# Kernel optimization log

Hardware: AMD Instinct MI355X
Metric: run time of the kernel (lower is better)

Reference implementation:

```python
import jax, jax.numpy as jnp
from jax import lax
import numpy as np

B, T, D, H, C = 256, 2048, 40, 128, 35
LN_EPS = 1e-5


def _uniform(key, shape, scale):
    return jax.random.uniform(key, shape, jnp.float32, -scale, scale)


def setup_inputs() -> dict:
    key = jax.random.key(0)
    ks = jax.random.split(key, 16)
    s = 1.0 / np.sqrt(H)  # PyTorch LSTM init scale
    inp = {
        "x": jax.random.normal(ks[0], (B, T, D), jnp.float32),
        "length": jax.random.randint(ks[1], (B,), 1, T + 1, jnp.int32),
        # layer 0 (input_size=D)
        "W_ih0": _uniform(ks[2], (4 * H, D), s),
        "W_hh0": _uniform(ks[3], (4 * H, H), s),
        "b_ih0": _uniform(ks[4], (4 * H,), s),
        "b_hh0": _uniform(ks[5], (4 * H,), s),
        # layer 1 (input_size=H)
        "W_ih1": _uniform(ks[6], (4 * H, H), s),
        "W_hh1": _uniform(ks[7], (4 * H, H), s),
        "b_ih1": _uniform(ks[8], (4 * H,), s),
        "b_hh1": _uniform(ks[9], (4 * H,), s),
        # LayerNorm + Linear head
        "ln_gamma": jnp.ones((H,), jnp.float32),
        "ln_beta": jnp.zeros((H,), jnp.float32),
        "fc_w": _uniform(ks[10], (C, H), 1.0 / np.sqrt(H)),
        "fc_b": _uniform(ks[11], (C,), 1.0 / np.sqrt(H)),
    }
    return inp


def _lstm_layer(xs, length, W_ih, W_hh, b_ih, b_hh):
    # xs: [T, B, D_in]; masked recurrence emulates pack_padded_sequence:
    # state is frozen for t >= length, so the final h equals the state at
    # each sequence's last valid step.
    Tn, Bn = xs.shape[0], xs.shape[1]
    Hn = W_hh.shape[1]
    h0 = jnp.zeros((Bn, Hn), xs.dtype)
    c0 = jnp.zeros((Bn, Hn), xs.dtype)

    def step(carry, inp):
        h, c = carry
        x_t, t = inp
        gates = x_t @ W_ih.T + b_ih + h @ W_hh.T + b_hh  # [B, 4H]
        i, f, g, o = jnp.split(gates, 4, axis=-1)  # PyTorch gate order i,f,g,o
        i = jax.nn.sigmoid(i)
        f = jax.nn.sigmoid(f)
        g = jnp.tanh(g)
        o = jax.nn.sigmoid(o)
        c_new = f * c + i * g
        h_new = o * jnp.tanh(c_new)
        m = (t < length)[:, None]
        h = jnp.where(m, h_new, h)
        c = jnp.where(m, c_new, c)
        return (h, c), h

    (h_fin, c_fin), hs = lax.scan(step, (h0, c0), (xs, jnp.arange(Tn)))
    return hs, h_fin


def reference(x, length, W_ih0, W_hh0, b_ih0, b_hh0, W_ih1, W_hh1, b_ih1, b_hh1,
              ln_gamma, ln_beta, fc_w, fc_b):
    xs = jnp.transpose(x, (1, 0, 2))  # [T, B, D]
    hs1, _ = _lstm_layer(xs, length, W_ih0, W_hh0, b_ih0, b_hh0)
    _, h_last = _lstm_layer(hs1, length, W_ih1, W_hh1, b_ih1, b_hh1)  # h[-1]: [B, H]
    # LayerNorm over feature dim
    mu = jnp.mean(h_last, axis=-1, keepdims=True)
    var = jnp.mean(jnp.square(h_last - mu), axis=-1, keepdims=True)
    hn = (h_last - mu) * lax.rsqrt(var + LN_EPS) * ln_gamma + ln_beta
    return hn @ fc_w.T + fc_b  # [B, C]
```

## Files before the change

kernel.cpp:

```cpp
#include <hip/hip_runtime.h>

#define Bn 256
#define Tn 2048
#define Dn 40
#define Hn 128
#define Cn 35

typedef _Float16 h2 __attribute__((ext_vector_type(2)));

__device__ __forceinline__ int sdot4(int a, int b, int c) {
#if __has_builtin(__builtin_amdgcn_sdot4)
  return __builtin_amdgcn_sdot4(a, b, c, false);
#else
  int r = c;
#pragma unroll
  for (int i = 0; i < 4; ++i)
    r += ((int)(a << (24 - 8 * i)) >> 24) * ((int)(b << (24 - 8 * i)) >> 24);
  return r;
#endif
}

__device__ __forceinline__ float fdot2f(h2 a, h2 b, float c) {
#if __has_builtin(__builtin_amdgcn_fdot2)
  return __builtin_amdgcn_fdot2(a, b, c, false);
#else
  return c + (float)(a[0]) * (float)(b[0]) + (float)(a[1]) * (float)(b[1]);
#endif
}

__device__ __forceinline__ h2 bch(int u) { return __builtin_bit_cast(h2, u); }

__device__ __forceinline__ int pk2i(float a, float b) {
  h2 r; r[0] = (_Float16)a; r[1] = (_Float16)b;
  return __builtin_bit_cast(int, r);
}

__device__ __forceinline__ float rcpf_(float x) {
#if __has_builtin(__builtin_amdgcn_rcpf)
  return __builtin_amdgcn_rcpf(x);
#else
  return 1.f / x;
#endif
}

__device__ __forceinline__ float sigm(float v) {
  v = fmaxf(fminf(v, 60.f), -60.f);
  return rcpf_(1.f + __expf(-v));
}

__device__ __forceinline__ float tanha(float v) {
  v = fmaxf(fminf(v, 15.f), -15.f);
  const float e = __expf(2.f * v);
  return (e - 1.f) * rcpf_(e + 1.f);
}

__device__ __forceinline__ int q8c(float v) {
  v = fminf(fmaxf(v, -127.f), 127.f);
  return (int)__builtin_rintf(v);
}

__device__ __forceinline__ int pk4(int a, int b, int c, int d) {
  return (a & 255) | ((b & 255) << 8) | ((c & 255) << 16) | (d << 24);
}

#if __has_builtin(__builtin_amdgcn_global_load_lds)
#define HAVE_GLDS 1
__device__ __forceinline__ void gl_lds16(const float* g, float* l) {
  __builtin_amdgcn_global_load_lds(
      (const __attribute__((address_space(1))) unsigned int*)(const void*)g,
      (__attribute__((address_space(3))) unsigned int*)(void*)l, 16, 0, 0);
}
#endif

__device__ __forceinline__ void quantW128(const float* __restrict__ p,
                                          int* __restrict__ q, float& sc) {
  float m = 1e-30f;
#pragma unroll
  for (int i = 0; i < 32; ++i) {
    const float4 v = reinterpret_cast<const float4*>(p)[i];
    m = fmaxf(m, fmaxf(fmaxf(fabsf(v.x), fabsf(v.y)),
                       fmaxf(fabsf(v.z), fabsf(v.w))));
  }
  const float inv = 127.f / m;
  sc = m * (1.f / 127.f);
#pragma unroll
  for (int i = 0; i < 32; ++i) {
    const float4 v = reinterpret_cast<const float4*>(p)[i];
    q[i] = pk4(q8c(v.x * inv), q8c(v.y * inv), q8c(v.z * inv), q8c(v.w * inv));
  }
}

#define RLST(w) __builtin_amdgcn_readlane(                                  \
    ((w) < 64 ? st0 : (w) < 128 ? st1 : (w) < 192 ? st2 : (w) < 256 ? st3  \
                                                        : st4), (w) & 63)

__global__ __launch_bounds__(512) void lstm2_fused(
    const float* __restrict__ x,
    const int*   __restrict__ length,
    const float* __restrict__ Wih0, const float* __restrict__ Whh0,
    const float* __restrict__ bih0, const float* __restrict__ bhh0,
    const float* __restrict__ Wih1, const float* __restrict__ Whh1,
    const float* __restrict__ bih1, const float* __restrict__ bhh1,
    const float* __restrict__ gam,  const float* __restrict__ bet,
    const float* __restrict__ fcw,  const float* __restrict__ fcb,
    float* __restrict__ out)
{
  __shared__ int   s_w0x[20][512];
  __shared__ __align__(16) float s_xraw[192 * 4];
  __shared__ int   s_xh2[2][320];
  __shared__ float s_xp[2][16][512];
  __shared__ float s_p0[4][132];
  __shared__ float s_p1[4][132];
  __shared__ int   s_hq[64];
  __shared__ float s_h1f[128];
  __shared__ float s_hn[128];

  const int tid  = threadIdx.x;
  const int lane = tid & 63;
  const int b    = blockIdx.x;
  const int len  = length[b];

  if (tid >= 256 && tid < 448) {
    const int seg0 = (tid >> 6) - 4;
    int seg = seg0 * 64 + lane;
    if (seg >= 160) seg = 0;
#if HAVE_GLDS
    gl_lds16(x + (size_t)b * Tn * Dn + seg * 4, &s_xraw[seg0 * 256]);
#else
    *(float4*)&s_xraw[seg * 4] =
        *(const float4*)(x + (size_t)b * Tn * Dn + seg * 4);
#endif
  }

  int q0h[32], q1x[32], q1h[32];
  float s0h, s1x, s1h;
  quantW128(Whh0 + (size_t)tid * Hn, q0h, s0h);
  quantW128(Wih1 + (size_t)tid * Hn, q1x, s1x);
  quantW128(Whh1 + (size_t)tid * Hn, q1h, s1h);
  s0h *= (1.f / 127.f);
  s1x *= (1.f / 127.f);
  s1h *= (1.f / 127.f);
  {
    const float* p = Wih0 + (size_t)tid * Dn;
#pragma unroll
    for (int k = 0; k < 20; ++k) s_w0x[k][tid] = pk2i(p[2 * k], p[2 * k + 1]);
  }
  const float bias0 = bih0[tid] + bhh0[tid];
  const float bias1 = bih1[tid] + bhh1[tid];

  float c0 = 0.f;
  float c1 = 0.f;

  if (tid < 64) s_hq[tid] = 0;
  __syncthreads();

  auto burst = [&](int bb) {
    const int* flat = &s_xh2[bb][0];
    const int st0 = flat[lane], st1 = flat[lane + 64], st2 = flat[lane + 128],
              st3 = flat[lane + 192], st4 = flat[lane + 256];
#pragma unroll
    for (int pass = 0; pass < 4; ++pass) {
      float a0 = 0.f, a1 = 0.f, a2 = 0.f, a3 = 0.f;
      const int r0 = pass * 4;
#pragma unroll
      for (int g = 0; g < 5; ++g) {
        const h2 w0 = bch(s_w0x[4 * g + 0][tid]);
        const h2 w1 = bch(s_w0x[4 * g + 1][tid]);
        const h2 w2 = bch(s_w0x[4 * g + 2][tid]);
        const h2 w3 = bch(s_w0x[4 * g + 3][tid]);
        a0 = fdot2f(bch(RLST(20 * (r0 + 0) + 4 * g + 0)), w0, a0);
        a0 = fdot2f(bch(RLST(20 * (r0 + 0) + 4 * g + 1)), w1, a0);
        a0 = fdot2f(bch(RLST(20 * (r0 + 0) + 4 * g + 2)), w2, a0);
        a0 = fdot2f(bch(RLST(20 * (r0 + 0) + 4 * g + 3)), w3, a0);
        a1 = fdot2f(bch(RLST(20 * (r0 + 1) + 4 * g + 0)), w0, a1);
        a1 = fdot2f(bch(RLST(20 * (r0 + 1) + 4 * g + 1)), w1, a1);
        a1 = fdot2f(bch(RLST(20 * (r0 + 1) + 4 * g + 2)), w2, a1);
        a1 = fdot2f(bch(RLST(20 * (r0 + 1) + 4 * g + 3)), w3, a1);
        a2 = fdot2f(bch(RLST(20 * (r0 + 2) + 4 * g + 0)), w0, a2);
        a2 = fdot2f(bch(RLST(20 * (r0 + 2) + 4 * g + 1)), w1, a2);
        a2 = fdot2f(bch(RLST(20 * (r0 + 2) + 4 * g + 2)), w2, a2);
        a2 = fdot2f(bch(RLST(20 * (r0 + 2) + 4 * g + 3)), w3, a2);
        a3 = fdot2f(bch(RLST(20 * (r0 + 3) + 4 * g + 0)), w0, a3);
        a3 = fdot2f(bch(RLST(20 * (r0 + 3) + 4 * g + 1)), w1, a3);
        a3 = fdot2f(bch(RLST(20 * (r0 + 3) + 4 * g + 2)), w2, a3);
        a3 = fdot2f(bch(RLST(20 * (r0 + 3) + 4 * g + 3)), w3, a3);
      }
      s_xp[bb][r0 + 0][tid] = a0;
      s_xp[bb][r0 + 1][tid] = a1;
      s_xp[bb][r0 + 2][tid] = a2;
      s_xp[bb][r0 + 3][tid] = a3;
    }
  };

  if (tid >= 256 && tid < 416) {
    const int u = tid - 256;
    const float4 v = *(const float4*)&s_xraw[4 * u];
    s_xh2[0][2 * u]     = pk2i(v.x, v.y);
    s_xh2[0][2 * u + 1] = pk2i(v.z, v.w);
  }
  __syncthreads();
  burst(0);
  __syncthreads();
  s_p0[tid >> 7][tid & 127] = bias0 + s_xp[0][0][tid];
  __syncthreads();

#pragma unroll 1
  for (int t = 0; t < len; ++t) {
    const int tl = t & 15;

    if (tid < 128) {
      const float gi = s_p0[0][tid], gf = s_p0[1][tid];
      const float gg = s_p0[2][tid], go = s_p0[3][tid];
      c0 = sigm(gf) * c0 + sigm(gi) * tanha(gg);
      const float h = sigm(go) * tanha(c0);
      ((signed char*)s_hq)[tid] = (signed char)(int)__builtin_rintf(h * 127.f);
    } else if (tid < 256) {
      if (t > 0) {
        const int u = tid - 128;
        const float gi = s_p1[0][u], gf = s_p1[1][u];
        const float gg = s_p1[2][u], go = s_p1[3][u];
        c1 = sigm(gf) * c1 + sigm(gi) * tanha(gg);
        const float h = sigm(go) * tanha(c1);
        ((signed char*)s_hq)[128 + u] =
            (signed char)(int)__builtin_rintf(h * 127.f);
      }
    } else if (tid < 416 && tl == 13) {
      const int u = tid - 256;
      const float4 v = *(const float4*)&s_xraw[4 * u];
      const int nb = ((t + 3) >> 4) & 1;
      s_xh2[nb][2 * u]     = pk2i(v.x, v.y);
      s_xh2[nb][2 * u + 1] = pk2i(v.z, v.w);
    }
    __syncthreads();

    const int vq = s_hq[lane];

    if (tid >= 256 && tid < 448 && tl == 12) {
      const int t0 = (t & ~15) + 16;
      if (t0 <= Tn - 16) {
        const int seg0 = (tid >> 6) - 4;
        int seg = seg0 * 64 + lane;
        if (seg >= 160) seg = 0;
#if HAVE_GLDS
        gl_lds16(x + ((size_t)b * Tn + t0) * Dn + seg * 4,
                 &s_xraw[seg0 * 256]);
#else
        *(float4*)&s_xraw[seg * 4] =
            *(const float4*)(x + ((size_t)b * Tn + t0) * Dn + seg * 4);
#endif
      }
    }

    const int rowi = t + 1;
    const float xacc = s_xp[(rowi >> 4) & 1][rowi & 15][tid];

    int ia = 0, ia2 = 0, ib = 0, ib2 = 0, ic = 0, ic2 = 0;
#pragma unroll
    for (int j = 0; j < 32; j += 2) {
      const int s0 = __builtin_amdgcn_readlane(vq, j);
      const int s1 = __builtin_amdgcn_readlane(vq, j + 1);
      ia  = sdot4(s0, q0h[j], ia);
      ib  = sdot4(s0, q1x[j], ib);
      ia2 = sdot4(s1, q0h[j + 1], ia2);
      ib2 = sdot4(s1, q1x[j + 1], ib2);
    }
#pragma unroll
    for (int j = 0; j < 32; j += 2) {
      const int s0 = __builtin_amdgcn_readlane(vq, 32 + j);
      const int s1 = __builtin_amdgcn_readlane(vq, 33 + j);
      ic  = sdot4(s0, q1h[j], ic);
      ic2 = sdot4(s1, q1h[j + 1], ic2);
    }
    s_p0[tid >> 7][tid & 127] = bias0 + xacc + (float)(ia + ia2) * s0h;
    s_p1[tid >> 7][tid & 127] =
        bias1 + (float)(ib + ib2) * s1x + (float)(ic + ic2) * s1h;

    if (tl == 14) burst(((t + 2) >> 4) & 1);
    __syncthreads();
  }

  if (tid >= 128 && tid < 256) {
    const int u = tid - 128;
    const float gi = s_p1[0][u], gf = s_p1[1][u];
    const float gg = s_p1[2][u], go = s_p1[3][u];
    c1 = sigm(gf) * c1 + sigm(gi) * tanha(gg);
    s_h1f[u] = sigm(go) * tanha(c1);
  }
  __syncthreads();

  if (tid < 64) {
    const float a = s_h1f[tid], d = s_h1f[64 + tid];
    float s = a + d, q = a * a + d * d;
#pragma unroll
    for (int m = 32; m >= 1; m >>= 1) {
      s += __shfl_xor(s, m, 64);
      q += __shfl_xor(q, m, 64);
    }
    const float mu = s * (1.f / 128.f);
    float var = q * (1.f / 128.f) - mu * mu;
    var = fmaxf(var, 0.f);
    const float rstd = rsqrtf(var + 1e-5f);
    s_hn[tid]      = (a - mu) * rstd * gam[tid]      + bet[tid];
    s_hn[64 + tid] = (d - mu) * rstd * gam[64 + tid] + bet[64 + tid];
  }
  __syncthreads();

  if (tid < Cn) {
    float acc = fcb[tid];
    const float* wp = fcw + tid * Hn;
#pragma unroll 4
    for (int k = 0; k < Hn; ++k) acc += s_hn[k] * wp[k];
    out[(size_t)b * Cn + tid] = acc;
  }
}

extern "C" void kernel_launch(void* const* d_in, const int* in_sizes, int n_in,
                              void* d_out, int out_size, void* d_ws, size_t ws_size,
                              hipStream_t stream) {
  (void)in_sizes; (void)n_in; (void)d_ws; (void)ws_size; (void)out_size;
  lstm2_fused<<<dim3(Bn), dim3(512), 0, stream>>>(
      (const float*)d_in[0],  (const int*)d_in[1],
      (const float*)d_in[2],  (const float*)d_in[3],
      (const float*)d_in[4],  (const float*)d_in[5],
      (const float*)d_in[6],  (const float*)d_in[7],
      (const float*)d_in[8],  (const float*)d_in[9],
      (const float*)d_in[10], (const float*)d_in[11],
      (const float*)d_in[12], (const float*)d_in[13],
      (float*)d_out);
}
```

Measured before the change: 2.512 ms.

## Replace per-step block barriers with wave-specialized pipeline using LDS flag polling

Restructures the fused two-layer LSTM so that each pair of waves owns one job: the layer-0 recurrence, the layer-1 recurrence, the layer-1 input projection, or the chunked x projection. Each wave computes all four gates for its hidden units in registers. The waves hand off through ring buffers in LDS and synchronize with published step counters that are polled, instead of two block-wide __syncthreads per timestep. This lets layer 1 run behind layer 0 in a software pipeline and takes the gate exchange through shared memory off the critical path. The cost is spin-polling overhead, more registers per wave, and subtle memory-ordering correctness risks around the flag protocol.

```diff
diff --git a/kernel.cpp b/kernel.cpp
--- a/kernel.cpp
+++ b/kernel.cpp
@@ -7,6 +7,9 @@
 #define Cn 35
 
 typedef _Float16 h2 __attribute__((ext_vector_type(2)));
+typedef int int4v __attribute__((ext_vector_type(4)));
+
+__device__ __forceinline__ int imin(int a, int b) { return a < b ? a : b; }
 
 __device__ __forceinline__ int sdot4(int a, int b, int c) {
 #if __has_builtin(__builtin_amdgcn_sdot4)
@@ -61,6 +64,13 @@
 
 __device__ __forceinline__ int pk4(int a, int b, int c, int d) {
   return (a & 255) | ((b & 255) << 8) | ((c & 255) << 16) | (d << 24);
+}
+
+__device__ __forceinline__ int dpp_x1(int v) {
+  return __builtin_amdgcn_update_dpp(0, v, 0xB1, 0xF, 0xF, true);
+}
+__device__ __forceinline__ int dpp_x2(int v) {
+  return __builtin_amdgcn_update_dpp(0, v, 0x4E, 0xF, 0xF, true);
 }
 
 #if __has_builtin(__builtin_amdgcn_global_load_lds)
@@ -94,7 +104,9 @@
     ((w) < 64 ? st0 : (w) < 128 ? st1 : (w) < 192 ? st2 : (w) < 256 ? st3  \
                                                         : st4), (w) & 63)
 
-__global__ __launch_bounds__(512) void lstm2_fused(
+#define MEMBAR() asm volatile("" ::: "memory")
+
+__global__ __launch_bounds__(512, 2) void lstm2_fused(
     const float* __restrict__ x,
     const int*   __restrict__ length,
     const float* __restrict__ Wih0, const float* __restrict__ Whh0,
@@ -105,187 +117,316 @@
     const float* __restrict__ fcw,  const float* __restrict__ fcb,
     float* __restrict__ out)
 {
-  __shared__ int   s_w0x[20][512];
-  __shared__ __align__(16) float s_xraw[192 * 4];
-  __shared__ int   s_xh2[2][320];
-  __shared__ float s_xp[2][16][512];
-  __shared__ float s_p0[4][132];
-  __shared__ float s_p1[4][132];
-  __shared__ int   s_hq[64];
+  __shared__ __align__(16) float s_xraw[160 * 4];
+  __shared__ int   s_xh2[320];
+  __shared__ float s_xp[2][16][8][64];
+  __shared__ float s_term[4][4][2][64];
+  __shared__ int   s_h0q[4][32];
+  __shared__ int   s_h1q[4][32];
+  __shared__ __align__(32) int s_flag[8];
   __shared__ float s_h1f[128];
   __shared__ float s_hn[128];
 
   const int tid  = threadIdx.x;
   const int lane = tid & 63;
+  const int wv   = tid >> 6;
   const int b    = blockIdx.x;
   const int len  = length[b];
 
-  if (tid >= 256 && tid < 448) {
-    const int seg0 = (tid >> 6) - 4;
-    int seg = seg0 * 64 + lane;
-    if (seg >= 160) seg = 0;
+  if (wv == 6) {
+    const float* xs = x + (size_t)b * Tn * Dn;
 #if HAVE_GLDS
-    gl_lds16(x + (size_t)b * Tn * Dn + seg * 4, &s_xraw[seg0 * 256]);
-#else
-    *(float4*)&s_xraw[seg * 4] =
-        *(const float4*)(x + (size_t)b * Tn * Dn + seg * 4);
-#endif
-  }
-
-  int q0h[32], q1x[32], q1h[32];
-  float s0h, s1x, s1h;
-  quantW128(Whh0 + (size_t)tid * Hn, q0h, s0h);
-  quantW128(Wih1 + (size_t)tid * Hn, q1x, s1x);
-  quantW128(Whh1 + (size_t)tid * Hn, q1h, s1h);
-  s0h *= (1.f / 127.f);
-  s1x *= (1.f / 127.f);
-  s1h *= (1.f / 127.f);
-  {
-    const float* p = Wih0 + (size_t)tid * Dn;
-#pragma unroll
-    for (int k = 0; k < 20; ++k) s_w0x[k][tid] = pk2i(p[2 * k], p[2 * k + 1]);
-  }
-  const float bias0 = bih0[tid] + bhh0[tid];
-  const float bias1 = bih1[tid] + bhh1[tid];
-
-  float c0 = 0.f;
-  float c1 = 0.f;
-
-  if (tid < 64) s_hq[tid] = 0;
+    gl_lds16(xs + lane * 4,        &s_xraw[0]);
+    gl_lds16(xs + (lane + 64) * 4, &s_xraw[256]);
+#else
+    *(float4*)&s_xraw[lane * 4] = *(const float4*)(xs + lane * 4);
+    *(float4*)&s_xraw[(lane + 64) * 4] = *(const float4*)(xs + (lane + 64) * 4);
+#endif
+  } else if (wv == 7 && lane < 32) {
+    const float* xs = x + (size_t)b * Tn * Dn;
+#if HAVE_GLDS
+    gl_lds16(xs + (lane + 128) * 4, &s_xraw[512]);
+#else
+    *(float4*)&s_xraw[(lane + 128) * 4] = *(const float4*)(xs + (lane + 128) * 4);
+#endif
+  }
+  if (tid < 128) { ((int*)s_h0q)[tid] = 0; ((int*)s_h1q)[tid] = 0; }
+  if (tid < 8) s_flag[tid] = 0;
   __syncthreads();
-
-  auto burst = [&](int bb) {
-    const int* flat = &s_xh2[bb][0];
-    const int st0 = flat[lane], st1 = flat[lane + 64], st2 = flat[lane + 128],
-              st3 = flat[lane + 192], st4 = flat[lane + 256];
-#pragma unroll
-    for (int pass = 0; pass < 4; ++pass) {
-      float a0 = 0.f, a1 = 0.f, a2 = 0.f, a3 = 0.f;
-      const int r0 = pass * 4;
-#pragma unroll
-      for (int g = 0; g < 5; ++g) {
-        const h2 w0 = bch(s_w0x[4 * g + 0][tid]);
-        const h2 w1 = bch(s_w0x[4 * g + 1][tid]);
-        const h2 w2 = bch(s_w0x[4 * g + 2][tid]);
-        const h2 w3 = bch(s_w0x[4 * g + 3][tid]);
-        a0 = fdot2f(bch(RLST(20 * (r0 + 0) + 4 * g + 0)), w0, a0);
-        a0 = fdot2f(bch(RLST(20 * (r0 + 0) + 4 * g + 1)), w1, a0);
-        a0 = fdot2f(bch(RLST(20 * (r0 + 0) + 4 * g + 2)), w2, a0);
-        a0 = fdot2f(bch(RLST(20 * (r0 + 0) + 4 * g + 3)), w3, a0);
-        a1 = fdot2f(bch(RLST(20 * (r0 + 1) + 4 * g + 0)), w0, a1);
-        a1 = fdot2f(bch(RLST(20 * (r0 + 1) + 4 * g + 1)), w1, a1);
-        a1 = fdot2f(bch(RLST(20 * (r0 + 1) + 4 * g + 2)), w2, a1);
-        a1 = fdot2f(bch(RLST(20 * (r0 + 1) + 4 * g + 3)), w3, a1);
-        a2 = fdot2f(bch(RLST(20 * (r0 + 2) + 4 * g + 0)), w0, a2);
-        a2 = fdot2f(bch(RLST(20 * (r0 + 2) + 4 * g + 1)), w1, a2);
-        a2 = fdot2f(bch(RLST(20 * (r0 + 2) + 4 * g + 2)), w2, a2);
-        a2 = fdot2f(bch(RLST(20 * (r0 + 2) + 4 * g + 3)), w3, a2);
-        a3 = fdot2f(bch(RLST(20 * (r0 + 3) + 4 * g + 0)), w0, a3);
-        a3 = fdot2f(bch(RLST(20 * (r0 + 3) + 4 * g + 1)), w1, a3);
-        a3 = fdot2f(bch(RLST(20 * (r0 + 3) + 4 * g + 2)), w2, a3);
-        a3 = fdot2f(bch(RLST(20 * (r0 + 3) + 4 * g + 3)), w3, a3);
-      }
-      s_xp[bb][r0 + 0][tid] = a0;
-      s_xp[bb][r0 + 1][tid] = a1;
-      s_xp[bb][r0 + 2][tid] = a2;
-      s_xp[bb][r0 + 3][tid] = a3;
-    }
-  };
-
-  if (tid >= 256 && tid < 416) {
-    const int u = tid - 256;
-    const float4 v = *(const float4*)&s_xraw[4 * u];
-    s_xh2[0][2 * u]     = pk2i(v.x, v.y);
-    s_xh2[0][2 * u + 1] = pk2i(v.z, v.w);
+  if (tid < 160) {
+    const float4 v = *(const float4*)&s_xraw[4 * tid];
+    s_xh2[2 * tid]     = pk2i(v.x, v.y);
+    s_xh2[2 * tid + 1] = pk2i(v.z, v.w);
   }
   __syncthreads();
-  burst(0);
-  __syncthreads();
-  s_p0[tid >> 7][tid & 127] = bias0 + s_xp[0][0][tid];
-  __syncthreads();
-
+
+  const __attribute__((address_space(3))) int* flagp3 =
+      (const __attribute__((address_space(3))) int*)(const void*)s_flag;
+  int4v f03 = {0, 0, 0, 0}, f47 = {0, 0, 0, 0};
+
+#define READFLAGS()                                                          \
+  asm volatile("ds_read_b128 %0, %2\n\tds_read_b128 %1, %2 offset:16\n\t"    \
+               "s_waitcnt lgkmcnt(0)"                                        \
+               : "=v"(f03), "=v"(f47) : "v"(flagp3) : "memory")
+#define PUBLISH(idx, val)                                                    \
+  do {                                                                       \
+    MEMBAR();                                                                \
+    asm volatile("s_waitcnt lgkmcnt(0)" ::: "memory");                       \
+    *(volatile int*)&s_flag[idx] = (val);                                    \
+  } while (0)
+#define POLL(COND)                                                           \
+  do {                                                                       \
+    if (!(COND)) {                                                           \
+      for (;;) {                                                             \
+        READFLAGS();                                                         \
+        if (COND) break;                                                     \
+        __builtin_amdgcn_s_sleep(1);                                         \
+      }                                                                      \
+    }                                                                        \
+    MEMBAR();                                                                \
+  } while (0)
+
+  if (wv < 2) {
+    const int half = wv;
+    const int u = (half << 6) | lane;
+    int qI[32], qF[32], qG[32], qO[32];
+    float sI, sF, sG, sO;
+    quantW128(Whh0 + (size_t)u * Hn, qI, sI);
+    quantW128(Whh0 + (size_t)(u + 128) * Hn, qF, sF);
+    quantW128(Whh0 + (size_t)(u + 256) * Hn, qG, sG);
+    quantW128(Whh0 + (size_t)(u + 384) * Hn, qO, sO);
+    sI *= (1.f / 127.f); sF *= (1.f / 127.f);
+    sG *= (1.f / 127.f); sO *= (1.f / 127.f);
+    const float bI = bih0[u]       + bhh0[u];
+    const float bF = bih0[u + 128] + bhh0[u + 128];
+    const float bG = bih0[u + 256] + bhh0[u + 256];
+    const float bO = bih0[u + 384] + bhh0[u + 384];
+    const int jo = half << 4, jp = (half ^ 1) << 4;
+    float c0 = 0.f;
+    int wA = 0;
 #pragma unroll 1
-  for (int t = 0; t < len; ++t) {
-    const int tl = t & 15;
-
-    if (tid < 128) {
-      const float gi = s_p0[0][tid], gf = s_p0[1][tid];
-      const float gg = s_p0[2][tid], go = s_p0[3][tid];
+    for (int t = 0; t < len; ++t) {
+      const int tl = t & 15;
+      POLL(f03[half ^ 1] >= t && imin(f47[0], f47[1]) >= t - 3 &&
+           (tl != 0 || imin(f47[2], f47[3]) >= 2 * (t >> 4) + 1));
+      const int pw = s_h0q[(t + 3) & 3][jp + (lane & 15)];
+      const int cs = (t >> 4) & 1;
+      const float xI = s_xp[cs][tl][half][lane];
+      const float xF = s_xp[cs][tl][half + 2][lane];
+      const float xG = s_xp[cs][tl][half + 4][lane];
+      const float xO = s_xp[cs][tl][half + 6][lane];
+      int aI = 0, aF = 0, aG = 0, aO = 0;
+      {
+        int sw[16];
+#pragma unroll
+        for (int j = 0; j < 16; ++j) sw[j] = __builtin_amdgcn_readlane(wA, 4 * j);
+#pragma unroll
+        for (int j = 0; j < 16; ++j) {
+          aI = sdot4(sw[j], qI[jo + j], aI); aF = sdot4(sw[j], qF[jo + j], aF);
+          aG = sdot4(sw[j], qG[jo + j], aG); aO = sdot4(sw[j], qO[jo + j], aO);
+        }
+#pragma unroll
+        for (int j = 0; j < 16; ++j) sw[j] = __builtin_amdgcn_readlane(pw, j);
+#pragma unroll
+        for (int j = 0; j < 16; ++j) {
+          aI = sdot4(sw[j], qI[jp + j], aI); aF = sdot4(sw[j], qF[jp + j], aF);
+          aG = sdot4(sw[j], qG[jp + j], aG); aO = sdot4(sw[j], qO[jp + j], aO);
+        }
+      }
+      const float gi = bI + xI + (float)aI * sI;
+      const float gf = bF + xF + (float)aF * sF;
+      const float gg = bG + xG + (float)aG * sG;
+      const float go = bO + xO + (float)aO * sO;
       c0 = sigm(gf) * c0 + sigm(gi) * tanha(gg);
       const float h = sigm(go) * tanha(c0);
-      ((signed char*)s_hq)[tid] = (signed char)(int)__builtin_rintf(h * 127.f);
-    } else if (tid < 256) {
-      if (t > 0) {
-        const int u = tid - 128;
-        const float gi = s_p1[0][u], gf = s_p1[1][u];
-        const float gg = s_p1[2][u], go = s_p1[3][u];
-        c1 = sigm(gf) * c1 + sigm(gi) * tanha(gg);
-        const float h = sigm(go) * tanha(c1);
-        ((signed char*)s_hq)[128 + u] =
-            (signed char)(int)__builtin_rintf(h * 127.f);
-      }
-    } else if (tid < 416 && tl == 13) {
-      const int u = tid - 256;
-      const float4 v = *(const float4*)&s_xraw[4 * u];
-      const int nb = ((t + 3) >> 4) & 1;
-      s_xh2[nb][2 * u]     = pk2i(v.x, v.y);
-      s_xh2[nb][2 * u + 1] = pk2i(v.z, v.w);
-    }
-    __syncthreads();
-
-    const int vq = s_hq[lane];
-
-    if (tid >= 256 && tid < 448 && tl == 12) {
-      const int t0 = (t & ~15) + 16;
-      if (t0 <= Tn - 16) {
-        const int seg0 = (tid >> 6) - 4;
-        int seg = seg0 * 64 + lane;
-        if (seg >= 160) seg = 0;
+      int v = (((int)__builtin_rintf(h * 127.f)) & 255) << (8 * (lane & 3));
+      v |= dpp_x1(v); v |= dpp_x2(v);
+      wA = v;
+      if ((lane & 3) == 0) s_h0q[t & 3][jo + (lane >> 2)] = v;
+      PUBLISH(wv, t + 1);
+      READFLAGS();
+    }
+  } else if (wv < 4) {
+    const int half = wv - 2;
+    const int u = (half << 6) | lane;
+    int qI[32], qF[32], qG[32], qO[32];
+    float sI, sF, sG, sO;
+    quantW128(Whh1 + (size_t)u * Hn, qI, sI);
+    quantW128(Whh1 + (size_t)(u + 128) * Hn, qF, sF);
+    quantW128(Whh1 + (size_t)(u + 256) * Hn, qG, sG);
+    quantW128(Whh1 + (size_t)(u + 384) * Hn, qO, sO);
+    sI *= (1.f / 127.f); sF *= (1.f / 127.f);
+    sG *= (1.f / 127.f); sO *= (1.f / 127.f);
+    const int jo = half << 4, jp = (half ^ 1) << 4;
+    float c1 = 0.f;
+    int wA = 0;
+#pragma unroll 1
+    for (int t = 0; t < len; ++t) {
+      POLL(f03[2 + (half ^ 1)] >= t && imin(f47[0], f47[1]) >= t + 1);
+      const int pw = s_h1q[(t + 3) & 3][jp + (lane & 15)];
+      const float tvI = s_term[t & 3][0][half][lane];
+      const float tvF = s_term[t & 3][1][half][lane];
+      const float tvG = s_term[t & 3][2][half][lane];
+      const float tvO = s_term[t & 3][3][half][lane];
+      int aI = 0, aF = 0, aG = 0, aO = 0;
+      {
+        int sw[16];
+#pragma unroll
+        for (int j = 0; j < 16; ++j) sw[j] = __builtin_amdgcn_readlane(wA, 4 * j);
+#pragma unroll
+        for (int j = 0; j < 16; ++j) {
+          aI = sdot4(sw[j], qI[jo + j], aI); aF = sdot4(sw[j], qF[jo + j], aF);
+          aG = sdot4(sw[j], qG[jo + j], aG); aO = sdot4(sw[j], qO[jo + j], aO);
+        }
+#pragma unroll
+        for (int j = 0; j < 16; ++j) sw[j] = __builtin_amdgcn_readlane(pw, j);
+#pragma unroll
+        for (int j = 0; j < 16; ++j) {
+          aI = sdot4(sw[j], qI[jp + j], aI); aF = sdot4(sw[j], qF[jp + j], aF);
+          aG = sdot4(sw[j], qG[jp + j], aG); aO = sdot4(sw[j], qO[jp + j], aO);
+        }
+      }
+      const float gi = tvI + (float)aI * sI;
+      const float gf = tvF + (float)aF * sF;
+      const float gg = tvG + (float)aG * sG;
+      const float go = tvO + (float)aO * sO;
+      c1 = sigm(gf) * c1 + sigm(gi) * tanha(gg);
+      const float h = sigm(go) * tanha(c1);
+      if (t == len - 1) s_h1f[u] = h;
+      int v = (((int)__builtin_rintf(h * 127.f)) & 255) << (8 * (lane & 3));
+      v |= dpp_x1(v); v |= dpp_x2(v);
+      wA = v;
+      if ((lane & 3) == 0) s_h1q[t & 3][jo + (lane >> 2)] = v;
+      PUBLISH(wv, t + 1);
+      READFLAGS();
+    }
+  } else if (wv < 6) {
+    const int half = wv - 4;
+    const int u = (half << 6) | lane;
+    int qI[32], qF[32], qG[32], qO[32];
+    float sI, sF, sG, sO;
+    quantW128(Wih1 + (size_t)u * Hn, qI, sI);
+    quantW128(Wih1 + (size_t)(u + 128) * Hn, qF, sF);
+    quantW128(Wih1 + (size_t)(u + 256) * Hn, qG, sG);
+    quantW128(Wih1 + (size_t)(u + 384) * Hn, qO, sO);
+    sI *= (1.f / 127.f); sF *= (1.f / 127.f);
+    sG *= (1.f / 127.f); sO *= (1.f / 127.f);
+    const float bI = bih1[u]       + bhh1[u];
+    const float bF = bih1[u + 128] + bhh1[u + 128];
+    const float bG = bih1[u + 256] + bhh1[u + 256];
+    const float bO = bih1[u + 384] + bhh1[u + 384];
+#pragma unroll 1
+    for (int t = 0; t < len; ++t) {
+      POLL(f03[0] >= t + 1 && f03[1] >= t + 1 &&
+           imin(f03[2], f03[3]) >= t - 3);
+      const int vq = s_h0q[t & 3][lane & 31];
+      int aI = 0, aF = 0, aG = 0, aO = 0;
+      {
+        int sw[32];
+#pragma unroll
+        for (int j = 0; j < 32; ++j) sw[j] = __builtin_amdgcn_readlane(vq, j);
+#pragma unroll
+        for (int j = 0; j < 32; ++j) {
+          aI = sdot4(sw[j], qI[j], aI); aF = sdot4(sw[j], qF[j], aF);
+          aG = sdot4(sw[j], qG[j], aG); aO = sdot4(sw[j], qO[j], aO);
+        }
+      }
+      s_term[t & 3][0][half][lane] = bI + (float)aI * sI;
+      s_term[t & 3][1][half][lane] = bF + (float)aF * sF;
+      s_term[t & 3][2][half][lane] = bG + (float)aG * sG;
+      s_term[t & 3][3][half][lane] = bO + (float)aO * sO;
+      PUBLISH(wv, t + 1);
+      READFLAGS();
+    }
+  } else {
+    const int half = wv - 6;
+    const int u = (half << 6) | lane;
+    int wpA[20], wpB[20], wpC[20], wpD[20];
+    {
+      const float* p;
+      p = Wih0 + (size_t)u * Dn;
+#pragma unroll
+      for (int w2 = 0; w2 < 20; ++w2) wpA[w2] = pk2i(p[2 * w2], p[2 * w2 + 1]);
+      p = Wih0 + (size_t)(u + 128) * Dn;
+#pragma unroll
+      for (int w2 = 0; w2 < 20; ++w2) wpB[w2] = pk2i(p[2 * w2], p[2 * w2 + 1]);
+      p = Wih0 + (size_t)(u + 256) * Dn;
+#pragma unroll
+      for (int w2 = 0; w2 < 20; ++w2) wpC[w2] = pk2i(p[2 * w2], p[2 * w2 + 1]);
+      p = Wih0 + (size_t)(u + 384) * Dn;
+#pragma unroll
+      for (int w2 = 0; w2 < 20; ++w2) wpD[w2] = pk2i(p[2 * w2], p[2 * w2 + 1]);
+    }
+    const int nch = (len + 15) >> 4;
+#pragma unroll 1
+    for (int k = 0; k < nch; ++k) {
+      const bool more = (k + 1 < nch);
+      if (more) {
+        const float* xs = x + ((size_t)b * Tn + (size_t)(k + 1) * 16) * Dn;
+        if (half == 0) {
 #if HAVE_GLDS
-        gl_lds16(x + ((size_t)b * Tn + t0) * Dn + seg * 4,
-                 &s_xraw[seg0 * 256]);
-#else
-        *(float4*)&s_xraw[seg * 4] =
-            *(const float4*)(x + ((size_t)b * Tn + t0) * Dn + seg * 4);
-#endif
-      }
-    }
-
-    const int rowi = t + 1;
-    const float xacc = s_xp[(rowi >> 4) & 1][rowi & 15][tid];
-
-    int ia = 0, ia2 = 0, ib = 0, ib2 = 0, ic = 0, ic2 = 0;
-#pragma unroll
-    for (int j = 0; j < 32; j += 2) {
-      const int s0 = __builtin_amdgcn_readlane(vq, j);
-      const int s1 = __builtin_amdgcn_readlane(vq, j + 1);
-      ia  = sdot4(s0, q0h[j], ia);
-      ib  = sdot4(s0, q1x[j], ib);
-      ia2 = sdot4(s1, q0h[j + 1], ia2);
-      ib2 = sdot4(s1, q1x[j + 1], ib2);
-    }
-#pragma unroll
-    for (int j = 0; j < 32; j += 2) {
-      const int s0 = __builtin_amdgcn_readlane(vq, 32 + j);
-      const int s1 = __builtin_amdgcn_readlane(vq, 33 + j);
-      ic  = sdot4(s0, q1h[j], ic);
-      ic2 = sdot4(s1, q1h[j + 1], ic2);
-    }
-    s_p0[tid >> 7][tid & 127] = bias0 + xacc + (float)(ia + ia2) * s0h;
-    s_p1[tid >> 7][tid & 127] =
-        bias1 + (float)(ib + ib2) * s1x + (float)(ic + ic2) * s1h;
-
-    if (tl == 14) burst(((t + 2) >> 4) & 1);
-    __syncthreads();
-  }
-
-  if (tid >= 128 && tid < 256) {
-    const int u = tid - 128;
-    const float gi = s_p1[0][u], gf = s_p1[1][u];
-    const float gg = s_p1[2][u], go = s_p1[3][u];
-    c1 = sigm(gf) * c1 + sigm(gi) * tanha(gg);
-    s_h1f[u] = sigm(go) * tanha(c1);
-  }
+          gl_lds16(xs + lane * 4,        &s_xraw[0]);
+          gl_lds16(xs + (lane + 64) * 4, &s_xraw[256]);
+#else
+          *(float4*)&s_xraw[lane * 4] = *(const float4*)(xs + lane * 4);
+          *(float4*)&s_xraw[(lane + 64) * 4] = *(const float4*)(xs + (lane + 64) * 4);
+#endif
+        } else if (lane < 32) {
+#if HAVE_GLDS
+          gl_lds16(xs + (lane + 128) * 4, &s_xraw[512]);
+#else
+          *(float4*)&s_xraw[(lane + 128) * 4] = *(const float4*)(xs + (lane + 128) * 4);
+#endif
+        }
+      }
+      POLL(f47[2 + (half ^ 1)] >= 2 * k);
+      {
+        const int* flat = s_xh2;
+        const int st0 = flat[lane], st1 = flat[lane + 64],
+                  st2 = flat[lane + 128], st3 = flat[lane + 192],
+                  st4 = flat[lane + 256];
+#pragma unroll 1
+        for (int tl = 0; tl < 16; ++tl) {
+          float a0 = 0.f, a1 = 0.f, a2 = 0.f, a3 = 0.f;
+#pragma unroll
+          for (int w2 = 0; w2 < 20; ++w2) {
+            const h2 s = bch(RLST(20 * tl + w2));
+            a0 = fdot2f(s, bch(wpA[w2]), a0);
+            a1 = fdot2f(s, bch(wpB[w2]), a1);
+            a2 = fdot2f(s, bch(wpC[w2]), a2);
+            a3 = fdot2f(s, bch(wpD[w2]), a3);
+          }
+          s_xp[k & 1][tl][half][lane]     = a0;
+          s_xp[k & 1][tl][half + 2][lane] = a1;
+          s_xp[k & 1][tl][half + 4][lane] = a2;
+          s_xp[k & 1][tl][half + 6][lane] = a3;
+        }
+      }
+      PUBLISH(wv, 2 * k + 1);
+      if (more) {
+        POLL(imin(f03[0], f03[1]) >= 16 * k &&
+             f47[2 + (half ^ 1)] >= 2 * k + 1);
+#if HAVE_GLDS
+        asm volatile("s_waitcnt vmcnt(0)" ::: "memory");
+#endif
+        if (half == 0) {
+          float4 v = *(const float4*)&s_xraw[4 * lane];
+          s_xh2[2 * lane] = pk2i(v.x, v.y);
+          s_xh2[2 * lane + 1] = pk2i(v.z, v.w);
+          v = *(const float4*)&s_xraw[4 * (lane + 64)];
+          s_xh2[2 * (lane + 64)] = pk2i(v.x, v.y);
+          s_xh2[2 * (lane + 64) + 1] = pk2i(v.z, v.w);
+        } else if (lane < 32) {
+          float4 v = *(const float4*)&s_xraw[4 * (lane + 128)];
+          s_xh2[2 * (lane + 128)] = pk2i(v.x, v.y);
+          s_xh2[2 * (lane + 128) + 1] = pk2i(v.z, v.w);
+        }
+      }
+      PUBLISH(wv, 2 * k + 2);
+      READFLAGS();
+    }
+  }
+
   __syncthreads();
 
   if (tid < 64) {
```

Result: slower. 5.348 ms (+112.9%).
